# Performance work log

Measured on AMD Instinct MI355X. Metric: run time of the kernel, lower is better.

Reference implementation:

```python
import jax, jax.numpy as jnp
import numpy as np
from jax import lax

BITW = 1
BITA = 3


def _ste_round(x, n):
    # round with straight-through gradient (Round -> Identity override)
    return x + lax.stop_gradient(jnp.round(x * n) / n - x)


def _quantize_active(x, bitA):
    # cabs: clip |x| to [0, 1], then k-bit uniform quantization with STE round
    x = jnp.minimum(1.0, jnp.abs(x))
    if bitA == 32:
        return x
    n = float(2 ** bitA - 1)
    return _ste_round(x, n)


def _quantize_weight(w, bitW):
    if bitW == 32:
        return w
    if bitW == 1:
        # sign with STE (Sign -> Identity): grad w.r.t. w is 1
        E = lax.stop_gradient(jnp.mean(jnp.abs(w)))
        y = w / E
        return (y + lax.stop_gradient(jnp.sign(y) - y)) * E
    n = float(2 ** bitW - 1)
    w = jnp.clip(w * 0.5 + 0.5, 0.0, 1.0)
    return 2.0 * _ste_round(w, n) - 1.0


def setup_inputs() -> dict:
    key = jax.random.key(0)
    kx, kw, kb = jax.random.split(key, 3)
    x = jax.random.normal(kx, (32, 56, 56, 256), dtype=jnp.float32)
    W = jax.random.normal(kw, (3, 3, 256, 256), dtype=jnp.float32) * 0.02  # HWIO
    b = jax.random.normal(kb, (256,), dtype=jnp.float32) * 0.01
    return {"x": x, "W": W, "b": b}


def reference(x, W, b):
    xq = _quantize_active(x, BITA)          # [N,H,W,C] quantized activations
    wq = _quantize_weight(W, BITW)          # [kh,kw,Cin,Cout] binarized weights
    out = lax.conv_general_dilated(
        xq, wq,
        window_strides=(1, 1),
        padding="SAME",
        dimension_numbers=("NHWC", "HWIO", "NHWC"),
    )
    return out + b  # act = identity
```

## Files before the change

### kernel.cpp

```cpp
#include <hip/hip_runtime.h>

typedef __attribute__((ext_vector_type(4))) int int4v;
typedef __attribute__((ext_vector_type(16))) int int16v;

#define NPIX 100352
#define PPIX 107648
#define KTAP 2304
#define LDK 144
#define BSZ (256 * LDK)

__global__ __launch_bounds__(256) void quant_w_kernel(const float* __restrict__ Wm,
                                                      signed char* __restrict__ Bt,
                                                      float* __restrict__ Esum) {
  __shared__ signed char sT[64][80];
  __shared__ float red[4];
  const int k0 = blockIdx.x * 64;
  const int c0 = blockIdx.y * 64;
  const int t = threadIdx.x;
  const int cc = t & 63;
  const int r0 = (t >> 6) * 16;
  float s = 0.f;
#pragma unroll
  for (int i = 0; i < 16; ++i) {
    const int k = r0 + i;
    float w = Wm[(long)(k0 + k) * 256 + c0 + cc];
    s += fabsf(w);
    sT[cc][k] = (signed char)((w > 0.f) ? 1 : ((w < 0.f) ? -1 : 0));
  }
#pragma unroll
  for (int o = 32; o > 0; o >>= 1) s += __shfl_down(s, o, 64);
  if ((t & 63) == 0) red[t >> 6] = s;
  __syncthreads();
  if (t == 0) atomicAdd(Esum, red[0] + red[1] + red[2] + red[3]);
  const int co = t >> 2;
  const int kc = (t & 3) * 16;
  int4v v = *(const int4v*)&sT[co][kc];
  *(int4v*)(Bt + (long)(c0 + co) * KTAP + k0 + kc) = v;
}

__global__ __launch_bounds__(256) void quant_x_kernel(const float* __restrict__ x,
                                                      signed char* __restrict__ xq) {
  const int tid = blockIdx.x * 256 + threadIdx.x;
  const int ci = tid & 63;
  const int pix = tid >> 6;
  const int q1 = pix / 58;
  const int wp = pix - q1 * 58;
  const int n = q1 / 58;
  const int hp = q1 - n * 58;
  unsigned int qv = 0;
  if ((unsigned)(hp - 1) < 56u && (unsigned)(wp - 1) < 56u) {
    const int src = n * 3136 + (hp - 1) * 56 + (wp - 1);
    float4 v = ((const float4*)x)[src * 64 + ci];
    qv  = (unsigned int)(int)rintf(fminf(1.f, fabsf(v.x)) * 7.f);
    qv |= ((unsigned int)(int)rintf(fminf(1.f, fabsf(v.y)) * 7.f)) << 8;
    qv |= ((unsigned int)(int)rintf(fminf(1.f, fabsf(v.z)) * 7.f)) << 16;
    qv |= ((unsigned int)(int)rintf(fminf(1.f, fabsf(v.w)) * 7.f)) << 24;
  }
  ((unsigned int*)xq)[tid] = qv;
}

__device__ __forceinline__ int tap_shift(int u) {
  const int tp = u >> 1;
  return ((tp / 3 - 1) * 58 + (tp % 3) - 1) * 256 + (u & 1) * 128;
}

__global__ __launch_bounds__(256, 2) void conv_kernel(const signed char* __restrict__ xq,
                                                      const signed char* __restrict__ Bt,
                                                      const float* __restrict__ bias,
                                                      const float* __restrict__ Esum,
                                                      float* __restrict__ out) {
  __shared__ signed char Bs[2 * BSZ];

  const int t = threadIdx.x;
  const int lane = t & 63;
  const int wid = t >> 6;
  const int bid = blockIdx.x;
  const int tile = (bid & 7) * 98 + (bid >> 3);
  const int m0 = tile * 128;
  const int wm = (wid & 1) * 64;
  const int wn = (wid >> 1) * 128;
  const int lrow = lane & 31;
  const int khalf = (lane >> 5) * 16;

  int pb0, pb1;
  {
    const int p0 = m0 + wm + lrow;
    const int n0 = p0 / 3136, r0 = p0 - n0 * 3136;
    const int h0 = r0 / 56, w0 = r0 - h0 * 56;
    pb0 = ((n0 * 58 + h0 + 1) * 58 + (w0 + 1)) * 256 + khalf;
    const int p1 = p0 + 32;
    const int n1 = p1 / 3136, r1 = p1 - n1 * 3136;
    const int h1 = r1 / 56, w1 = r1 - h1 * 56;
    pb1 = ((n1 * 58 + h1 + 1) * 58 + (w1 + 1)) * 256 + khalf;
  }

  const int brow = t >> 3;
  const int bcol = (t & 7) * 16;
  const int gb = brow * KTAP + bcol;
  const int lb = brow * LDK + bcol;

  int16v acc[2][4];
#pragma unroll
  for (int a = 0; a < 2; ++a)
#pragma unroll
    for (int b = 0; b < 4; ++b)
#pragma unroll
      for (int r = 0; r < 16; ++r) acc[a][b][r] = 0;

  int4v raA0 = *(const int4v*)(xq + pb0 + tap_shift(0));
  int4v raA1 = *(const int4v*)(xq + pb1 + tap_shift(0));
  int4v rb[8];
#pragma unroll
  for (int i = 0; i < 8; ++i) rb[i] = *(const int4v*)(Bt + gb + i * (32 * KTAP));
#pragma unroll
  for (int i = 0; i < 8; ++i) *(int4v*)(Bs + lb + i * (32 * LDK)) = rb[i];
#pragma unroll
  for (int i = 0; i < 8; ++i) rb[i] = *(const int4v*)(Bt + gb + 128 + i * (32 * KTAP));
  asm volatile("s_waitcnt lgkmcnt(0)" ::: "memory");
  __builtin_amdgcn_s_barrier();
  __builtin_amdgcn_sched_barrier(0);

  for (int s = 0; s < 18; ++s) {
    const int ash = tap_shift(s);
    const int ashN = tap_shift(s < 17 ? s + 1 : 17);
    signed char* Bcur = Bs + (s & 1) * BSZ;
    signed char* Bnxt = Bs + ((~s) & 1) * BSZ;
    const signed char* a0p = xq + pb0 + ash;
    const signed char* a1p = xq + pb1 + ash;
    const signed char* n0p = xq + pb0 + ashN;
    const signed char* n1p = xq + pb1 + ashN;

    if (s + 1 < 18) {
#pragma unroll
      for (int i = 0; i < 8; ++i) *(int4v*)(Bnxt + lb + i * (32 * LDK)) = rb[i];
    }
    if (s + 2 < 18) {
      const int ko2 = (s + 2) * 128;
#pragma unroll
      for (int i = 0; i < 8; ++i) rb[i] = *(const int4v*)(Bt + gb + ko2 + i * (32 * KTAP));
    }

#pragma unroll
    for (int ks = 0; ks < 4; ++ks) {
      int4v nx0 = *(const int4v*)((ks < 3) ? (a0p + (ks + 1) * 32) : n0p);
      int4v nx1 = *(const int4v*)((ks < 3) ? (a1p + (ks + 1) * 32) : n1p);
      const int ko = ks * 32 + khalf;
      int4v b0 = *(const int4v*)(Bcur + (wn + lrow) * LDK + ko);
      int4v b1 = *(const int4v*)(Bcur + (wn + 32 + lrow) * LDK + ko);
      int4v b2 = *(const int4v*)(Bcur + (wn + 64 + lrow) * LDK + ko);
      int4v b3 = *(const int4v*)(Bcur + (wn + 96 + lrow) * LDK + ko);
      __builtin_amdgcn_s_setprio(1);
      acc[0][0] = __builtin_amdgcn_mfma_i32_32x32x32_i8(raA0, b0, acc[0][0], 0, 0, 0);
      acc[0][1] = __builtin_amdgcn_mfma_i32_32x32x32_i8(raA0, b1, acc[0][1], 0, 0, 0);
      acc[0][2] = __builtin_amdgcn_mfma_i32_32x32x32_i8(raA0, b2, acc[0][2], 0, 0, 0);
      acc[0][3] = __builtin_amdgcn_mfma_i32_32x32x32_i8(raA0, b3, acc[0][3], 0, 0, 0);
      acc[1][0] = __builtin_amdgcn_mfma_i32_32x32x32_i8(raA1, b0, acc[1][0], 0, 0, 0);
      acc[1][1] = __builtin_amdgcn_mfma_i32_32x32x32_i8(raA1, b1, acc[1][1], 0, 0, 0);
      acc[1][2] = __builtin_amdgcn_mfma_i32_32x32x32_i8(raA1, b2, acc[1][2], 0, 0, 0);
      acc[1][3] = __builtin_amdgcn_mfma_i32_32x32x32_i8(raA1, b3, acc[1][3], 0, 0, 0);
      __builtin_amdgcn_s_setprio(0);
      raA0 = nx0; raA1 = nx1;
    }

    if (s < 17) {
      asm volatile("s_waitcnt lgkmcnt(0)" ::: "memory");
      __builtin_amdgcn_sched_barrier(0);
      __builtin_amdgcn_s_barrier();
      __builtin_amdgcn_sched_barrier(0);
    }
  }

  const float scale = Esum[0] * (1.0f / (589824.0f * 7.0f));
#pragma unroll
  for (int mt = 0; mt < 2; ++mt)
#pragma unroll
    for (int nt = 0; nt < 4; ++nt) {
      const int col = wn + nt * 32 + lrow;
      const float bv = bias[col];
#pragma unroll
      for (int r = 0; r < 16; ++r) {
        const int row = (r & 3) + 8 * (r >> 2) + 4 * (lane >> 5);
        const int m = m0 + wm + mt * 32 + row;
        out[(long)m * 256 + col] = (float)acc[mt][nt][r] * scale + bv;
      }
    }
}

extern "C" void kernel_launch(void* const* d_in, const int* in_sizes, int n_in,
                              void* d_out, int out_size, void* d_ws, size_t ws_size,
                              hipStream_t stream) {
  const float* x    = (const float*)d_in[0];
  const float* Wm   = (const float*)d_in[1];
  const float* bias = (const float*)d_in[2];
  float* out = (float*)d_out;

  float* Esum = (float*)d_ws;
  signed char* Bt = (signed char*)d_ws + 256;
  signed char* xq = (signed char*)d_ws + 256 + 589824;

  hipMemsetAsync(d_ws, 0, 4, stream);
  quant_w_kernel<<<dim3(36, 4), 256, 0, stream>>>(Wm, Bt, Esum);
  quant_x_kernel<<<26912, 256, 0, stream>>>(x, xq);
  conv_kernel<<<784, 256, 0, stream>>>(xq, Bt, bias, Esum, out);
}
```

Measured before the change: 271.7 us.

## Store quantized activations channel-chunk-major so conv A loads coalesce

Quantized activations are now stored as 16 channel-chunk planes, each holding 16 bytes per padded pixel, instead of pixel-major rows of 256 bytes. The quant kernel writes one 16-byte chunk per thread per plane, and the conv kernel computes A addresses from a plane index plus pixel offset. Adjacent lanes that read neighbouring pixels now touch contiguous 16-byte segments, which is meant to make the A-operand global loads coalesce better. The cost is that the quant kernel reads strided 64-byte chunks of x and writes to 16 separate planes.

Result: faster. 265.3 us (-2.4%).

```diff
diff --git a/kernel.cpp b/kernel.cpp
--- a/kernel.cpp
+++ b/kernel.cpp
@@ -8,6 +8,7 @@
 #define KTAP 2304
 #define LDK 144
 #define BSZ (256 * LDK)
+#define CHB (PPIX * 16)
 
 __global__ __launch_bounds__(256) void quant_w_kernel(const float* __restrict__ Wm,
                                                       signed char* __restrict__ Bt,
@@ -39,32 +40,34 @@
 }
 
 __global__ __launch_bounds__(256) void quant_x_kernel(const float* __restrict__ x,
-                                                      signed char* __restrict__ xq) {
-  const int tid = blockIdx.x * 256 + threadIdx.x;
-  const int ci = tid & 63;
-  const int pix = tid >> 6;
+                                                      signed char* __restrict__ xqT) {
+  const int pix = blockIdx.x * 256 + threadIdx.x;
+  if (pix >= PPIX) return;
+  const int c = blockIdx.y;
   const int q1 = pix / 58;
   const int wp = pix - q1 * 58;
-  const int n = q1 / 58;
+  const int n  = q1 / 58;
   const int hp = q1 - n * 58;
-  unsigned int qv = 0;
+  int4v out = {0, 0, 0, 0};
   if ((unsigned)(hp - 1) < 56u && (unsigned)(wp - 1) < 56u) {
     const int src = n * 3136 + (hp - 1) * 56 + (wp - 1);
-    float4 v = ((const float4*)x)[src * 64 + ci];
-    qv  = (unsigned int)(int)rintf(fminf(1.f, fabsf(v.x)) * 7.f);
-    qv |= ((unsigned int)(int)rintf(fminf(1.f, fabsf(v.y)) * 7.f)) << 8;
-    qv |= ((unsigned int)(int)rintf(fminf(1.f, fabsf(v.z)) * 7.f)) << 16;
-    qv |= ((unsigned int)(int)rintf(fminf(1.f, fabsf(v.w)) * 7.f)) << 24;
-  }
-  ((unsigned int*)xq)[tid] = qv;
-}
-
-__device__ __forceinline__ int tap_shift(int u) {
-  const int tp = u >> 1;
-  return ((tp / 3 - 1) * 58 + (tp % 3) - 1) * 256 + (u & 1) * 128;
-}
-
-__global__ __launch_bounds__(256, 2) void conv_kernel(const signed char* __restrict__ xq,
+    const float4* px = (const float4*)(x + (long)src * 256 + c * 16);
+#pragma unroll
+    for (int j = 0; j < 4; ++j) {
+      float4 v = px[j];
+      unsigned q;
+      q  = (unsigned)(int)rintf(fminf(1.f, fabsf(v.x)) * 7.f);
+      q |= ((unsigned)(int)rintf(fminf(1.f, fabsf(v.y)) * 7.f)) << 8;
+      q |= ((unsigned)(int)rintf(fminf(1.f, fabsf(v.z)) * 7.f)) << 16;
+      q |= ((unsigned)(int)rintf(fminf(1.f, fabsf(v.w)) * 7.f)) << 24;
+      out[j] = (int)q;
+    }
+  }
+  *(int4v*)(xqT + (long)c * CHB + pix * 16) = out;
+}
+
+
+__global__ __launch_bounds__(256, 2) void conv_kernel(const signed char* __restrict__ xqT,
                                                       const signed char* __restrict__ Bt,
                                                       const float* __restrict__ bias,
                                                       const float* __restrict__ Esum,
@@ -80,19 +83,26 @@
   const int wm = (wid & 1) * 64;
   const int wn = (wid >> 1) * 128;
   const int lrow = lane & 31;
-  const int khalf = (lane >> 5) * 16;
-
-  int pb0, pb1;
+  const int half = lane >> 5;
+
+  int pp0, pp1;
   {
     const int p0 = m0 + wm + lrow;
     const int n0 = p0 / 3136, r0 = p0 - n0 * 3136;
     const int h0 = r0 / 56, w0 = r0 - h0 * 56;
-    pb0 = ((n0 * 58 + h0 + 1) * 58 + (w0 + 1)) * 256 + khalf;
+    pp0 = (n0 * 58 + h0 + 1) * 58 + (w0 + 1);
     const int p1 = p0 + 32;
     const int n1 = p1 / 3136, r1 = p1 - n1 * 3136;
     const int h1 = r1 / 56, w1 = r1 - h1 * 56;
-    pb1 = ((n1 * 58 + h1 + 1) * 58 + (w1 + 1)) * 256 + khalf;
-  }
+    pp1 = (n1 * 58 + h1 + 1) * 58 + (w1 + 1);
+  }
+
+  auto aptr = [&](int u, int pp) -> const signed char* {
+    const int tp = u >> 1;
+    const int dp = (tp / 3 - 1) * 58 + (tp % 3) - 1;
+    return xqT + (((u & 1) * 8 + half) * PPIX + pp + dp) * 16;
+  };
+  const int ks_step = 2 * CHB;
 
   const int brow = t >> 3;
   const int bcol = (t & 7) * 16;
@@ -107,8 +117,8 @@
 #pragma unroll
       for (int r = 0; r < 16; ++r) acc[a][b][r] = 0;
 
-  int4v raA0 = *(const int4v*)(xq + pb0 + tap_shift(0));
-  int4v raA1 = *(const int4v*)(xq + pb1 + tap_shift(0));
+  int4v raA0 = *(const int4v*)aptr(0, pp0);
+  int4v raA1 = *(const int4v*)aptr(0, pp1);
   int4v rb[8];
 #pragma unroll
   for (int i = 0; i < 8; ++i) rb[i] = *(const int4v*)(Bt + gb + i * (32 * KTAP));
@@ -121,14 +131,12 @@
   __builtin_amdgcn_sched_barrier(0);
 
   for (int s = 0; s < 18; ++s) {
-    const int ash = tap_shift(s);
-    const int ashN = tap_shift(s < 17 ? s + 1 : 17);
     signed char* Bcur = Bs + (s & 1) * BSZ;
     signed char* Bnxt = Bs + ((~s) & 1) * BSZ;
-    const signed char* a0p = xq + pb0 + ash;
-    const signed char* a1p = xq + pb1 + ash;
-    const signed char* n0p = xq + pb0 + ashN;
-    const signed char* n1p = xq + pb1 + ashN;
+    const signed char* a0p = aptr(s, pp0);
+    const signed char* a1p = aptr(s, pp1);
+    const signed char* n0p = aptr(s < 17 ? s + 1 : 17, pp0);
+    const signed char* n1p = aptr(s < 17 ? s + 1 : 17, pp1);
 
     if (s + 1 < 18) {
 #pragma unroll
@@ -142,9 +150,9 @@
 
 #pragma unroll
     for (int ks = 0; ks < 4; ++ks) {
-      int4v nx0 = *(const int4v*)((ks < 3) ? (a0p + (ks + 1) * 32) : n0p);
-      int4v nx1 = *(const int4v*)((ks < 3) ? (a1p + (ks + 1) * 32) : n1p);
-      const int ko = ks * 32 + khalf;
+      int4v nx0 = *(const int4v*)((ks < 3) ? (a0p + (ks + 1) * ks_step) : n0p);
+      int4v nx1 = *(const int4v*)((ks < 3) ? (a1p + (ks + 1) * ks_step) : n1p);
+      const int ko = ks * 32 + half * 16;
       int4v b0 = *(const int4v*)(Bcur + (wn + lrow) * LDK + ko);
       int4v b1 = *(const int4v*)(Bcur + (wn + 32 + lrow) * LDK + ko);
       int4v b2 = *(const int4v*)(Bcur + (wn + 64 + lrow) * LDK + ko);
@@ -196,10 +204,10 @@
 
   float* Esum = (float*)d_ws;
   signed char* Bt = (signed char*)d_ws + 256;
-  signed char* xq = (signed char*)d_ws + 256 + 589824;
+  signed char* xqT = (signed char*)d_ws + 256 + 589824;
 
   hipMemsetAsync(d_ws, 0, 4, stream);
   quant_w_kernel<<<dim3(36, 4), 256, 0, stream>>>(Wm, Bt, Esum);
-  quant_x_kernel<<<26912, 256, 0, stream>>>(x, xq);
-  conv_kernel<<<784, 256, 0, stream>>>(xq, Bt, bias, Esum, out);
-}
+  quant_x_kernel<<<dim3(421, 16), 256, 0, stream>>>(x, xqT);
+  conv_kernel<<<784, 256, 0, stream>>>(xqT, Bt, bias, Esum, out);
+}
```
